# Kernel tuning notes

Measured on AMD Instinct MI355X. Metric: run time of the kernel, lower is better.

## Reference

```python
import jax, jax.numpy as jnp
import numpy as np

H = 4          # num attention heads
C1 = 64        # channel_num[0]
C2 = 128       # channel_num[1]
KV = C1 + C2   # 192
MLP = C1 * 4   # expand_ratio=4


def _layernorm(x, g, b, eps=1e-6):
    m = jnp.mean(x, axis=-1, keepdims=True)
    v = jnp.mean((x - m) ** 2, axis=-1, keepdims=True)
    return (x - m) * jax.lax.rsqrt(v + eps) * g + b


def setup_inputs() -> dict:
    key = jax.random.key(0)
    ks = jax.random.split(key, 12)
    B, N = 8, 3136
    s_q = 1.0 / np.sqrt(C1)
    s_kv = 1.0 / np.sqrt(KV)
    return {
        "emb1": jax.random.normal(ks[0], (B, N, C1), jnp.float32),
        "emb2": jax.random.normal(ks[1], (B, N, C2), jnp.float32),
        # per-head projection weights (nn.Linear convention: y = x @ W.T)
        "Wq": jax.random.uniform(ks[2], (H, C1, C1), jnp.float32, -s_q, s_q),
        "Wk": jax.random.uniform(ks[3], (H, KV, KV), jnp.float32, -s_kv, s_kv),
        "Wv": jax.random.uniform(ks[4], (H, KV, KV), jnp.float32, -s_kv, s_kv),
        "Wout": jax.random.uniform(ks[5], (C1, C1), jnp.float32, -s_q, s_q),
        "ln1_g": jnp.ones((C1,), jnp.float32),
        "ln1_b": jnp.zeros((C1,), jnp.float32),
        "lnall_g": jnp.ones((KV,), jnp.float32),
        "lnall_b": jnp.zeros((KV,), jnp.float32),
        "ffn_g": jnp.ones((C1,), jnp.float32),
        "ffn_b": jnp.zeros((C1,), jnp.float32),
        "fc1_w": jax.random.uniform(ks[6], (MLP, C1), jnp.float32, -s_q, s_q),
        "fc1_b": jnp.zeros((MLP,), jnp.float32),
        "fc2_w": jax.random.uniform(ks[7], (C1, MLP), jnp.float32, -1.0 / np.sqrt(MLP), 1.0 / np.sqrt(MLP)),
        "fc2_b": jnp.zeros((C1,), jnp.float32),
    }


def reference(emb1, emb2, Wq, Wk, Wv, Wout, ln1_g, ln1_b, lnall_g, lnall_b,
              ffn_g, ffn_b, fc1_w, fc1_b, fc2_w, fc2_b):
    # emb1: [B,N,C1], emb2: [B,N,C2]
    emb_all = jnp.concatenate([emb1, emb2], axis=2)          # [B,N,KV]
    cx1 = _layernorm(emb1, ln1_g, ln1_b)                     # [B,N,C1]
    ea = _layernorm(emb_all, lnall_g, lnall_b)               # [B,N,KV]

    # batched per-head projections (replaces Python loop over ModuleList)
    qT = jnp.einsum('bnc,hdc->bhdn', cx1, Wq)                # [B,H,C1,N]
    k = jnp.einsum('bnk,hdk->bhnd', ea, Wk)                  # [B,H,N,KV]
    vT = jnp.einsum('bnk,hdk->bhdn', ea, Wv)                 # [B,H,KV,N]

    scores = jnp.einsum('bhcn,bhnk->bhck', qT, k) / np.sqrt(KV)  # [B,H,C1,KV]
    # InstanceNorm2d over spatial dims (C1, KV) per (batch, head), affine=False
    m = jnp.mean(scores, axis=(2, 3), keepdims=True)
    v = jnp.mean((scores - m) ** 2, axis=(2, 3), keepdims=True)
    scores = (scores - m) * jax.lax.rsqrt(v + 1e-5)
    probs = jax.nn.softmax(scores, axis=3)                   # softmax over KV

    ctx = jnp.einsum('bhck,bhkn->bhcn', probs, vT)           # [B,H,C1,N]
    ctx = jnp.mean(ctx, axis=1).transpose(0, 2, 1)           # mean over heads -> [B,N,C1]
    o = ctx @ Wout.T                                         # [B,N,C1]

    cx = emb1 + o                                            # residual
    x = _layernorm(cx, ffn_g, ffn_b)
    x = jax.nn.gelu(x @ fc1_w.T + fc1_b, approximate=False)
    x = x @ fc2_w.T + fc2_b
    return x + cx
```

## Files before the change

kernel.cpp:

```cpp
#include <hip/hip_runtime.h>
#include <hip/hip_bf16.h>

typedef __hip_bfloat16 bf;
typedef unsigned short ushort_t;
typedef __attribute__((ext_vector_type(8))) short short8;
typedef __attribute__((ext_vector_type(4))) float f32x4;

#define NB 8
#define SEQ 3136
#define HD 4

__device__ __forceinline__ float lo_bf(unsigned u){ return __uint_as_float(u << 16); }
__device__ __forceinline__ float hi_bf(unsigned u){ return __uint_as_float(u & 0xffff0000u); }
__device__ __forceinline__ float b16f(ushort_t s){ return __uint_as_float(((unsigned)s) << 16); }
__device__ __forceinline__ unsigned short f2bfbits(float f){
  unsigned u = __float_as_uint(f);
  unsigned r = u + 0x7fffu + ((u >> 16) & 1u);
  return (unsigned short)(r >> 16);
}
__device__ __forceinline__ float ldin(const void* p, long i, bool isbf){
  return isbf ? __bfloat162float(((const bf*)p)[i]) : ((const float*)p)[i];
}
__device__ __forceinline__ float4 ld4(const void* p, long i, bool isbf){
  if (isbf){
    uint2 u = *reinterpret_cast<const uint2*>((const unsigned short*)p + i);
    return make_float4(lo_bf(u.x), hi_bf(u.x), lo_bf(u.y), hi_bf(u.y));
  }
  const float* f = (const float*)p + i;
  return make_float4(f[0], f[1], f[2], f[3]);
}
__device__ __forceinline__ short8 ldfrag(const void* p, long i, bool isbf){
  if (isbf) return *reinterpret_cast<const short8*>((const unsigned short*)p + i);
  const float* f = (const float*)p + i;
  short8 r;
  #pragma unroll
  for (int q=0;q<8;++q) r[q] = (short)f2bfbits(f[q]);
  return r;
}
#define DTYPE_FLAG(p) (((const unsigned*)(p))[0] == 0x3F803F80u)

__device__ __forceinline__ float wsum(float v){
  #pragma unroll
  for (int o = 32; o > 0; o >>= 1) v += __shfl_xor(v, o, 64);
  return v;
}
__device__ __forceinline__ float wmax(float v){
  #pragma unroll
  for (int o = 32; o > 0; o >>= 1) v = fmaxf(v, __shfl_xor(v, o, 64));
  return v;
}
__device__ __forceinline__ float gelu_f(float v){
  float u = v*(0.7978845608f + 0.0356774081f*v*v);
  return v * __builtin_amdgcn_rcpf(1.f + __expf(-2.f*u));
}

__global__ __launch_bounds__(256) void k_g(
    const void* __restrict__ emb1, const void* __restrict__ emb2,
    const void* __restrict__ g1, const void* __restrict__ b1,
    const void* __restrict__ ga, const void* __restrict__ ba,
    ushort_t* __restrict__ part, ushort_t* __restrict__ eag){
  bool isbf = DTYPE_FLAG(g1);
  __shared__ __align__(16) ushort_t z1t[64*40];
  __shared__ __align__(16) ushort_t zat[192*40];
  int tid = threadIdx.x, wave = tid >> 6, lane = tid & 63;
  int quad = lane >> 4, nl = lane & 15;
  int b = blockIdx.y, ch = blockIdx.x;
  long t0 = (long)b*SEQ + ch*32;
  float g1l = ldin(g1,lane,isbf), b1l = ldin(b1,lane,isbf);
  float ga0 = ldin(ga,lane,isbf),     ba0 = ldin(ba,lane,isbf);
  float ga1 = ldin(ga,64+lane,isbf),  ba1 = ldin(ba,64+lane,isbf);
  float ga2 = ldin(ga,128+lane,isbf), ba2 = ldin(ba,128+lane,isbf);
  #pragma unroll
  for (int k = 0; k < 8; ++k){
    int tok = wave*8 + k;
    long t = t0 + tok;
    float e1  = ldin(emb1, t*64 + lane, isbf);
    float e2a = ldin(emb2, t*128 + lane, isbf);
    float e2b = ldin(emb2, t*128 + 64 + lane, isbf);
    float s1 = wsum(e1), ss1 = wsum(e1*e1);
    float m1 = s1*(1.f/64.f);
    float r1 = rsqrtf(fmaxf(ss1*(1.f/64.f) - m1*m1, 0.f) + 1e-6f);
    z1t[lane*40 + tok] = f2bfbits((e1 - m1)*r1*g1l + b1l);
    float s23 = wsum(e2a+e2b), ss23 = wsum(e2a*e2a + e2b*e2b);
    float ma = (s1+s23)*(1.f/192.f);
    float ra = rsqrtf(fmaxf((ss1+ss23)*(1.f/192.f) - ma*ma, 0.f) + 1e-6f);
    unsigned short za0 = f2bfbits((e1  - ma)*ra*ga0 + ba0);
    unsigned short za1 = f2bfbits((e2a - ma)*ra*ga1 + ba1);
    unsigned short za2 = f2bfbits((e2b - ma)*ra*ga2 + ba2);
    zat[lane*40 + tok]       = za0;
    zat[(64+lane)*40 + tok]  = za1;
    zat[(128+lane)*40 + tok] = za2;
    eag[t*192 + lane]       = za0;
    eag[t*192 + 64 + lane]  = za1;
    eag[t*192 + 128 + lane] = za2;
  }
  __syncthreads();
  short8 a0 = *reinterpret_cast<const short8*>(&z1t[(wave*16+nl)*40 + quad*8]);
  ushort_t* P = part + ((long)b*98 + ch)*12288;
  #pragma unroll
  for (int nt = 0; nt < 12; ++nt){
    f32x4 cd = {0.f,0.f,0.f,0.f};
    short8 b0 = *reinterpret_cast<const short8*>(&zat[(nt*16+nl)*40 + quad*8]);
    cd = __builtin_amdgcn_mfma_f32_16x16x32_bf16(a0, b0, cd, 0, 0, 0);
    #pragma unroll
    for (int reg = 0; reg < 4; ++reg)
      P[(wave*16 + quad*4 + reg)*192 + nt*16 + nl] = f2bfbits(cd[reg]);
  }
}

__global__ __launch_bounds__(64) void k_red(
    const ushort_t* __restrict__ part, float* __restrict__ G){
  int idx4 = blockIdx.x*64 + threadIdx.x;
  int b = idx4 / 3072, e4 = idx4 - b*3072;
  const ushort_t* p = part + (long)b*98*12288 + e4*4;
  float s0=0.f, s1=0.f, s2=0.f, s3=0.f;
  #pragma unroll 2
  for (int ch = 0; ch < 98; ++ch){
    uint2 u = *reinterpret_cast<const uint2*>(p + (long)ch*12288);
    s0 += lo_bf(u.x); s1 += hi_bf(u.x); s2 += lo_bf(u.y); s3 += hi_bf(u.y);
  }
  ((float4*)G)[idx4] = make_float4(s0,s1,s2,s3);
}

__global__ __launch_bounds__(256) void k_s(
    const float* __restrict__ G, const void* __restrict__ Wq, const void* __restrict__ Wk,
    const void* __restrict__ lng, float* __restrict__ S){
  bool isbf = DTYPE_FLAG(lng);
  __shared__ __align__(16) ushort_t sGb[64*200];
  __shared__ __align__(16) ushort_t sT[48*72];
  int ec = blockIdx.x, h = blockIdx.y, b = blockIdx.z;
  int e0 = ec*48;
  int tid = threadIdx.x, wave = tid >> 6, lane = tid & 63;
  int quad = lane >> 4, nl = lane & 15;
  const float4* Gb4 = (const float4*)(G + (long)b*12288);
  for (int i16 = tid; i16 < 3072; i16 += 256){
    float4 v = Gb4[i16];
    int e = i16*4; int c = e/192, j = e - c*192;
    unsigned lo = (unsigned)f2bfbits(v.x) | ((unsigned)f2bfbits(v.y) << 16);
    unsigned hi = (unsigned)f2bfbits(v.z) | ((unsigned)f2bfbits(v.w) << 16);
    *reinterpret_cast<uint2*>(&sGb[c*200 + j]) = make_uint2(lo, hi);
  }
  __syncthreads();
  long wk0 = (long)h*36864;
  short8 aG[6];
  #pragma unroll
  for (int ks = 0; ks < 6; ++ks)
    aG[ks] = *reinterpret_cast<const short8*>(&sGb[(wave*16+nl)*200 + ks*32 + quad*8]);
  #pragma unroll
  for (int nt = 0; nt < 3; ++nt){
    f32x4 cd = {0.f,0.f,0.f,0.f};
    #pragma unroll
    for (int ks = 0; ks < 6; ++ks){
      short8 bw = ldfrag(Wk, wk0 + (long)(e0 + nt*16+nl)*192 + ks*32 + quad*8, isbf);
      cd = __builtin_amdgcn_mfma_f32_16x16x32_bf16(aG[ks], bw, cd, 0, 0, 0);
    }
    #pragma unroll
    for (int reg = 0; reg < 4; ++reg)
      sT[(nt*16+nl)*72 + wave*16 + quad*4 + reg] = f2bfbits(cd[reg]);
  }
  __syncthreads();
  long wq0 = (long)h*4096;
  short8 aQ[2];
  #pragma unroll
  for (int ks = 0; ks < 2; ++ks)
    aQ[ks] = ldfrag(Wq, wq0 + (long)(wave*16+nl)*64 + ks*32 + quad*8, isbf);
  const float scale = 0.07216878364870323f;
  float* Sb = S + ((long)b*HD + h)*12288;
  #pragma unroll
  for (int nt = 0; nt < 3; ++nt){
    f32x4 cd = {0.f,0.f,0.f,0.f};
    #pragma unroll
    for (int ks = 0; ks < 2; ++ks){
      short8 bt = *reinterpret_cast<const short8*>(&sT[(nt*16+nl)*72 + ks*32 + quad*8]);
      cd = __builtin_amdgcn_mfma_f32_16x16x32_bf16(aQ[ks], bt, cd, 0, 0, 0);
    }
    #pragma unroll
    for (int reg = 0; reg < 4; ++reg)
      Sb[(wave*16 + quad*4 + reg)*192 + e0 + nt*16 + nl] = cd[reg]*scale;
  }
}

__global__ __launch_bounds__(256) void k_smpv(
    const float* __restrict__ S, const void* __restrict__ Wv,
    const void* __restrict__ lng, float* __restrict__ Mh){
  bool isbf = DTYPE_FLAG(lng);
  __shared__ __align__(16) float sP[64*196];
  __shared__ __align__(16) unsigned sWv[192*52];
  __shared__ float red[8];
  __shared__ float stat[2];
  int jc = blockIdx.x, h = blockIdx.y, b = blockIdx.z;
  const float* Sb = S + ((long)b*HD + h)*12288;
  int tid = threadIdx.x, wave = tid >> 6, lane = tid & 63;
  long wv0 = (long)h*36864;
  float ps = 0.f, pss = 0.f;
  const float4* Sb4 = (const float4*)Sb;
  for (int i16 = tid; i16 < 3072; i16 += 256){
    float4 v = Sb4[i16];
    int e = i16*4; int c = e/192, j = e - c*192;
    *reinterpret_cast<float4*>(&sP[c*196 + j]) = v;
    ps += v.x + v.y + v.z + v.w;
    pss += v.x*v.x + v.y*v.y + v.z*v.z + v.w*v.w;
  }
  if (isbf){
    const unsigned short* wvp = (const unsigned short*)Wv + wv0 + jc*96;
    for (int idx = tid; idx < 4608; idx += 256){
      int r = idx/24, c2 = idx - r*24;
      uint2 v = *reinterpret_cast<const uint2*>(wvp + (long)r*192 + c2*4);
      *reinterpret_cast<uint2*>(&sWv[r*52 + c2*2]) = v;
    }
  } else {
    for (int idx = tid; idx < 9216; idx += 256){
      int r = idx/48, c = idx - r*48;
      float a0 = ldin(Wv, wv0 + (long)r*192 + jc*96 + c*2,     false);
      float a1 = ldin(Wv, wv0 + (long)r*192 + jc*96 + c*2 + 1, false);
      sWv[r*52 + c] = (unsigned)f2bfbits(a0) | ((unsigned)f2bfbits(a1) << 16);
    }
  }
  ps = wsum(ps); pss = wsum(pss);
  if (lane == 0){ red[wave] = ps; red[4+wave] = pss; }
  __syncthreads();
  if (tid == 0){
    float s  = red[0]+red[1]+red[2]+red[3];
    float s2 = red[4]+red[5]+red[6]+red[7];
    float m = s * (1.f/12288.f);
    stat[0] = m;
    stat[1] = rsqrtf(fmaxf(s2*(1.f/12288.f) - m*m, 0.f) + 1e-5f);
  }
  __syncthreads();
  float m = stat[0], r = stat[1];
  for (int rr = 0; rr < 16; ++rr){
    int row = wave*16 + rr;
    float v0 = (sP[row*196+lane]     - m)*r;
    float v1 = (sP[row*196+64+lane]  - m)*r;
    float v2 = (sP[row*196+128+lane] - m)*r;
    float mx = wmax(fmaxf(v0, fmaxf(v1, v2)));
    float e0 = __expf(v0-mx), e1 = __expf(v1-mx), e2 = __expf(v2-mx);
    float inv = 1.f / wsum(e0+e1+e2);
    sP[row*196+lane]     = e0*inv;
    sP[row*196+64+lane]  = e1*inv;
    sP[row*196+128+lane] = e2*inv;
  }
  __syncthreads();
  int ty = tid >> 4, tx = tid & 15;
  int j0 = jc*96 + tx*6;
  float acc[4][6];
  #pragma unroll
  for (int i=0;i<4;++i) for (int q=0;q<6;++q) acc[i][q]=0.f;
  #pragma unroll 2
  for (int e = 0; e < 192; ++e){
    float p4[4];
    #pragma unroll
    for (int i=0;i<4;++i) p4[i] = sP[(ty*4+i)*196 + e];
    unsigned wa = sWv[e*52 + tx*3];
    unsigned wb = sWv[e*52 + tx*3 + 1];
    unsigned wc = sWv[e*52 + tx*3 + 2];
    float w0 = lo_bf(wa), w1 = hi_bf(wa), w2 = lo_bf(wb),
          w3 = hi_bf(wb), w4 = lo_bf(wc), w5 = hi_bf(wc);
    #pragma unroll
    for (int i=0;i<4;++i){
      acc[i][0] = fmaf(p4[i], w0, acc[i][0]);
      acc[i][1] = fmaf(p4[i], w1, acc[i][1]);
      acc[i][2] = fmaf(p4[i], w2, acc[i][2]);
      acc[i][3] = fmaf(p4[i], w3, acc[i][3]);
      acc[i][4] = fmaf(p4[i], w4, acc[i][4]);
      acc[i][5] = fmaf(p4[i], w5, acc[i][5]);
    }
  }
  float* Mb = Mh + ((long)b*HD + h)*12288;
  #pragma unroll
  for (int i=0;i<4;++i)
    #pragma unroll
    for (int q=0;q<6;++q)
      Mb[(ty*4+i)*192 + j0 + q] = acc[i][q];
}

__global__ __launch_bounds__(256) void k_w2(
    const float* __restrict__ Mh, const void* __restrict__ Wout,
    const void* __restrict__ lng, ushort_t* __restrict__ W2){
  bool isbf = DTYPE_FLAG(lng);
  __shared__ __align__(16) float sM[64*49];
  int jc = blockIdx.x, b = blockIdx.y;
  int tid = threadIdx.x;
  for (int idx = tid; idx < 3072; idx += 256){
    int c = idx/48, j = idx - c*48;
    long base = (long)b*HD*12288 + c*192 + jc*48 + j;
    float s = Mh[base] + Mh[base+12288] + Mh[base+2*12288] + Mh[base+3*12288];
    sM[c*49 + j] = 0.25f*s;
  }
  __syncthreads();
  int ty = tid >> 4, tx = tid & 15;
  float acc[4][3];
  #pragma unroll
  for (int i=0;i<4;++i) for (int q=0;q<3;++q) acc[i][q]=0.f;
  for (int c = 0; c < 64; c += 4){
    float4 w4[4];
    #pragma unroll
    for (int i=0;i<4;++i) w4[i] = ld4(Wout, (long)(ty*4+i)*64 + c, isbf);
    float ww[4][4];
    #pragma unroll
    for (int i=0;i<4;++i){ ww[i][0]=w4[i].x; ww[i][1]=w4[i].y; ww[i][2]=w4[i].z; ww[i][3]=w4[i].w; }
    #pragma unroll
    for (int u = 0; u < 4; ++u){
      float t3[3];
      #pragma unroll
      for (int q=0;q<3;++q) t3[q] = sM[(c+u)*49 + tx*3 + q];
      #pragma unroll
      for (int i=0;i<4;++i)
        #pragma unroll
        for (int q=0;q<3;++q) acc[i][q] = fmaf(ww[i][u], t3[q], acc[i][q]);
    }
  }
  ushort_t* W2b = W2 + (long)b*12288;
  #pragma unroll
  for (int i=0;i<4;++i)
    #pragma unroll
    for (int q=0;q<3;++q)
      W2b[(ty*4+i)*192 + jc*48 + tx*3 + q] = f2bfbits(acc[i][q]);
}

__global__ __launch_bounds__(256) void k_tail(
    const void* __restrict__ emb1, const ushort_t* __restrict__ eag,
    const ushort_t* __restrict__ W2g,
    const void* __restrict__ ffg, const void* __restrict__ ffb,
    const void* __restrict__ f1w, const void* __restrict__ f1b,
    const void* __restrict__ f2w, const void* __restrict__ f2b,
    const void* __restrict__ lng, void* __restrict__ out){
  bool isbf = DTYPE_FLAG(lng);
  __shared__ __align__(16) ushort_t sCX[32*72];
  __shared__ __align__(16) ushort_t sX[32*88];
  __shared__ __align__(16) ushort_t sH[32*280];
  int tid = threadIdx.x, wave = tid >> 6, lane = tid & 63;
  int quad = lane >> 4, nl = lane & 15;
  int b = blockIdx.y;
  long tbase = (long)b*SEQ + blockIdx.x*32;

  short8 aO[2][6];
  #pragma unroll
  for (int tt = 0; tt < 2; ++tt)
    #pragma unroll
    for (int kt = 0; kt < 6; ++kt)
      aO[tt][kt] = *reinterpret_cast<const short8*>(eag + (tbase + tt*16 + nl)*192 + kt*32 + quad*8);
  const ushort_t* W2b = W2g + (long)b*12288;
  short8 bW[6];
  #pragma unroll
  for (int kt = 0; kt < 6; ++kt)
    bW[kt] = *reinterpret_cast<const short8*>(W2b + (wave*16+nl)*192 + kt*32 + quad*8);
  short8 bF1[8];
  #pragma unroll
  for (int nn = 0; nn < 4; ++nn)
    #pragma unroll
    for (int kt = 0; kt < 2; ++kt)
      bF1[nn*2+kt] = ldfrag(f1w, (long)((wave*4+nn)*16+nl)*64 + kt*32 + quad*8, isbf);
  short8 bF2[8];
  #pragma unroll
  for (int kt = 0; kt < 8; ++kt)
    bF2[kt] = ldfrag(f2w, (long)(wave*16+nl)*256 + kt*32 + quad*8, isbf);
  float e1v[2][4];
  #pragma unroll
  for (int tt = 0; tt < 2; ++tt)
    #pragma unroll
    for (int reg = 0; reg < 4; ++reg)
      e1v[tt][reg] = ldin(emb1, (tbase + tt*16 + quad*4 + reg)*64 + wave*16 + nl, isbf);
  float gl = ldin(ffg, lane, isbf), bl = ldin(ffb, lane, isbf);
  float f1bb[4];
  #pragma unroll
  for (int nn = 0; nn < 4; ++nn) f1bb[nn] = ldin(f1b, (wave*4+nn)*16+nl, isbf);
  float f2bb = ldin(f2b, wave*16+nl, isbf);

  #pragma unroll
  for (int tt = 0; tt < 2; ++tt){
    f32x4 cd = {0.f,0.f,0.f,0.f};
    #pragma unroll
    for (int kt = 0; kt < 6; ++kt)
      cd = __builtin_amdgcn_mfma_f32_16x16x32_bf16(aO[tt][kt], bW[kt], cd, 0, 0, 0);
    #pragma unroll
    for (int reg = 0; reg < 4; ++reg){
      int tokl = tt*16 + quad*4 + reg;
      sCX[tokl*72 + wave*16 + nl] = f2bfbits(cd[reg] + e1v[tt][reg]);
    }
  }
  __syncthreads();

  #pragma unroll
  for (int k = 0; k < 8; ++k){
    int tokl = wave*8 + k;
    float c = b16f(sCX[tokl*72 + lane]);
    float s = wsum(c), ss = wsum(c*c);
    float m = s*(1.f/64.f);
    float r = rsqrtf(fmaxf(ss*(1.f/64.f) - m*m, 0.f) + 1e-6f);
    sX[tokl*88 + lane] = f2bfbits((c - m)*r*gl + bl);
  }
  __syncthreads();

  short8 aX[2][2];
  #pragma unroll
  for (int tt = 0; tt < 2; ++tt)
    #pragma unroll
    for (int kt = 0; kt < 2; ++kt)
      aX[tt][kt] = *reinterpret_cast<const short8*>(&sX[(tt*16+nl)*88 + kt*32 + quad*8]);
  #pragma unroll
  for (int tt = 0; tt < 2; ++tt){
    #pragma unroll
    for (int nn = 0; nn < 4; ++nn){
      int nt = wave*4 + nn;
      f32x4 cd = {0.f,0.f,0.f,0.f};
      #pragma unroll
      for (int kt = 0; kt < 2; ++kt)
        cd = __builtin_amdgcn_mfma_f32_16x16x32_bf16(aX[tt][kt], bF1[nn*2+kt], cd, 0, 0, 0);
      #pragma unroll
      for (int reg = 0; reg < 4; ++reg)
        sH[(tt*16 + quad*4 + reg)*280 + nt*16 + nl] = f2bfbits(gelu_f(cd[reg] + f1bb[nn]));
    }
  }
  __syncthreads();

  short8 aH[2][8];
  #pragma unroll
  for (int tt = 0; tt < 2; ++tt)
    #pragma unroll
    for (int kt = 0; kt < 8; ++kt)
      aH[tt][kt] = *reinterpret_cast<const short8*>(&sH[(tt*16+nl)*280 + kt*32 + quad*8]);
  #pragma unroll
  for (int tt = 0; tt < 2; ++tt){
    f32x4 cd = {0.f,0.f,0.f,0.f};
    #pragma unroll
    for (int kt = 0; kt < 8; ++kt)
      cd = __builtin_amdgcn_mfma_f32_16x16x32_bf16(aH[tt][kt], bF2[kt], cd, 0, 0, 0);
    #pragma unroll
    for (int reg = 0; reg < 4; ++reg){
      int tokl = tt*16 + quad*4 + reg;
      int chn = wave*16 + nl;
      float y = cd[reg] + f2bb + b16f(sCX[tokl*72 + chn]);
      if (isbf) sCX[tokl*72 + chn] = f2bfbits(y);
      else ((float*)out)[(tbase + tokl)*64 + chn] = y;
    }
  }
  if (isbf){
    __syncthreads();
    #pragma unroll
    for (int pp = 0; pp < 2; ++pp){
      int tokl = wave*8 + pp*4 + (lane >> 4), prt = lane & 15;
      uint2 v = *reinterpret_cast<const uint2*>(&sCX[tokl*72 + prt*4]);
      *reinterpret_cast<uint2*>((ushort_t*)out + (tbase + tokl)*64 + prt*4) = v;
    }
  }
}

extern "C" void kernel_launch(void* const* d_in, const int* in_sizes, int n_in,
                              void* d_out, int out_size, void* d_ws, size_t ws_size,
                              hipStream_t stream){
  const void* emb1 = d_in[0];
  const void* emb2 = d_in[1];
  const void* Wq   = d_in[2];
  const void* Wk   = d_in[3];
  const void* Wv   = d_in[4];
  const void* Wout = d_in[5];
  const void* ln1g = d_in[6];
  const void* ln1b = d_in[7];
  const void* lag  = d_in[8];
  const void* lab  = d_in[9];
  const void* ffg  = d_in[10];
  const void* ffb  = d_in[11];
  const void* f1w  = d_in[12];
  const void* f1b  = d_in[13];
  const void* f2w  = d_in[14];
  const void* f2b  = d_in[15];

  char* base = (char*)d_ws;
  ushort_t* part = (ushort_t*)base;
  ushort_t* ea   = (ushort_t*)(base + 19267584);
  float*    G    = (float*)(base + 28901376);
  float*    S    = (float*)(base + 29294592);
  float*    Mh   = (float*)(base + 30867456);
  ushort_t* W2   = (ushort_t*)(base + 32440320);

  k_g   <<<dim3(98,NB),   256, 0, stream>>>(emb1, emb2, ln1g, ln1b, lag, lab, part, ea);
  k_red <<<384,            64, 0, stream>>>(part, G);
  k_s   <<<dim3(4,HD,NB), 256, 0, stream>>>(G, Wq, Wk, ln1g, S);
  k_smpv<<<dim3(2,HD,NB), 256, 0, stream>>>(S, Wv, ln1g, Mh);
  k_w2  <<<dim3(4,NB),    256, 0, stream>>>(Mh, Wout, ln1g, W2);
  k_tail<<<dim3(98,NB),   256, 0, stream>>>(emb1, ea, W2, ffg, ffb,
                                            f1w, f1b, f2w, f2b, ln1g, d_out);
}
```

Before: 211.7 us.

## Fuse all stages into one cooperative persistent kernel with grid syncs

Replaces six separate kernel launches with a single cooperative kernel of 512 blocks that runs each stage in turn, separated by grid-wide barriers, and keeps the old multi-kernel path as a fallback if the cooperative launch fails. The Gram-partial stage also now covers 64 tokens per block instead of 32, which halves the partial buffer and the reduction work. The goal is to remove launch gaps and the inter-kernel drain between the small middle stages. In exchange, the tail stage runs on 512 persistent blocks looping over 784 tiles, so the work is unevenly split, and the 64KB static shared allocation may limit occupancy and make the grid syncs costly.

```diff
diff --git a/kernel.cpp b/kernel.cpp
--- a/kernel.cpp
+++ b/kernel.cpp
@@ -1,5 +1,7 @@
 #include <hip/hip_runtime.h>
 #include <hip/hip_bf16.h>
+#include <hip/hip_cooperative_groups.h>
+namespace cg = cooperative_groups;
 
 typedef __hip_bfloat16 bf;
 typedef unsigned short ushort_t;
@@ -54,25 +56,419 @@
   return v * __builtin_amdgcn_rcpf(1.f + __expf(-2.f*u));
 }
 
+__global__ __launch_bounds__(256) void k_all(
+    const void* __restrict__ emb1, const void* __restrict__ emb2,
+    const void* __restrict__ Wq,   const void* __restrict__ Wk,
+    const void* __restrict__ Wv,   const void* __restrict__ Wout,
+    const void* __restrict__ ln1g, const void* __restrict__ ln1b,
+    const void* __restrict__ lag,  const void* __restrict__ lab,
+    const void* __restrict__ ffg,  const void* __restrict__ ffb,
+    const void* __restrict__ f1w,  const void* __restrict__ f1b,
+    const void* __restrict__ f2w,  const void* __restrict__ f2b,
+    ushort_t* __restrict__ part, ushort_t* __restrict__ eag,
+    float* __restrict__ G, float* __restrict__ S, float* __restrict__ Mh,
+    ushort_t* __restrict__ W2, void* __restrict__ out){
+  cg::grid_group grid = cg::this_grid();
+  bool isbf = DTYPE_FLAG(ln1g);
+  __shared__ __align__(16) unsigned char smem[65536];
+  __shared__ float red[8];
+  __shared__ float stat[2];
+  int bid = blockIdx.x;
+  int tid = threadIdx.x, wave = tid >> 6, lane = tid & 63;
+  int quad = lane >> 4, nl = lane & 15;
+
+  if (bid < 392){
+    ushort_t* z1t = (ushort_t*)smem;
+    ushort_t* zat = (ushort_t*)(smem + 9216);
+    int ch = bid % 49, b = bid / 49;
+    long t0 = (long)b*SEQ + ch*64;
+    float g1l = ldin(ln1g,lane,isbf), b1l = ldin(ln1b,lane,isbf);
+    float ga0 = ldin(lag,lane,isbf),     ba0 = ldin(lab,lane,isbf);
+    float ga1 = ldin(lag,64+lane,isbf),  ba1 = ldin(lab,64+lane,isbf);
+    float ga2 = ldin(lag,128+lane,isbf), ba2 = ldin(lab,128+lane,isbf);
+    #pragma unroll 4
+    for (int k = 0; k < 16; ++k){
+      int tok = wave*16 + k;
+      long t = t0 + tok;
+      float e1  = ldin(emb1, t*64 + lane, isbf);
+      float e2a = ldin(emb2, t*128 + lane, isbf);
+      float e2b = ldin(emb2, t*128 + 64 + lane, isbf);
+      float s1 = wsum(e1), ss1 = wsum(e1*e1);
+      float m1 = s1*(1.f/64.f);
+      float r1 = rsqrtf(fmaxf(ss1*(1.f/64.f) - m1*m1, 0.f) + 1e-6f);
+      z1t[lane*72 + tok] = f2bfbits((e1 - m1)*r1*g1l + b1l);
+      float s23 = wsum(e2a+e2b), ss23 = wsum(e2a*e2a + e2b*e2b);
+      float ma = (s1+s23)*(1.f/192.f);
+      float ra = rsqrtf(fmaxf((ss1+ss23)*(1.f/192.f) - ma*ma, 0.f) + 1e-6f);
+      unsigned short za0 = f2bfbits((e1  - ma)*ra*ga0 + ba0);
+      unsigned short za1 = f2bfbits((e2a - ma)*ra*ga1 + ba1);
+      unsigned short za2 = f2bfbits((e2b - ma)*ra*ga2 + ba2);
+      zat[lane*72 + tok]       = za0;
+      zat[(64+lane)*72 + tok]  = za1;
+      zat[(128+lane)*72 + tok] = za2;
+      eag[t*192 + lane]       = za0;
+      eag[t*192 + 64 + lane]  = za1;
+      eag[t*192 + 128 + lane] = za2;
+    }
+    __syncthreads();
+    short8 a0 = *reinterpret_cast<const short8*>(&z1t[(wave*16+nl)*72 + quad*8]);
+    short8 a1 = *reinterpret_cast<const short8*>(&z1t[(wave*16+nl)*72 + 32 + quad*8]);
+    ushort_t* P = part + ((long)b*49 + ch)*12288;
+    #pragma unroll
+    for (int nt = 0; nt < 12; ++nt){
+      f32x4 cd = {0.f,0.f,0.f,0.f};
+      short8 b0 = *reinterpret_cast<const short8*>(&zat[(nt*16+nl)*72 + quad*8]);
+      cd = __builtin_amdgcn_mfma_f32_16x16x32_bf16(a0, b0, cd, 0, 0, 0);
+      short8 b1v = *reinterpret_cast<const short8*>(&zat[(nt*16+nl)*72 + 32 + quad*8]);
+      cd = __builtin_amdgcn_mfma_f32_16x16x32_bf16(a1, b1v, cd, 0, 0, 0);
+      #pragma unroll
+      for (int reg = 0; reg < 4; ++reg)
+        P[(wave*16 + quad*4 + reg)*192 + nt*16 + nl] = f2bfbits(cd[reg]);
+    }
+  }
+  grid.sync();
+
+  {
+    int idx4 = bid*256 + tid;
+    if (idx4 < 24576){
+      int b = idx4 / 3072, e4 = idx4 - b*3072;
+      const ushort_t* p = part + (long)b*49*12288 + e4*4;
+      float s0=0.f, s1=0.f, s2=0.f, s3=0.f;
+      #pragma unroll
+      for (int ch = 0; ch < 49; ++ch){
+        uint2 u = *reinterpret_cast<const uint2*>(p + (long)ch*12288);
+        s0 += lo_bf(u.x); s1 += hi_bf(u.x); s2 += lo_bf(u.y); s3 += hi_bf(u.y);
+      }
+      ((float4*)G)[idx4] = make_float4(s0,s1,s2,s3);
+    }
+  }
+  grid.sync();
+
+  if (bid < 128){
+    ushort_t* sGb = (ushort_t*)smem;
+    ushort_t* sT  = (ushort_t*)(smem + 25600);
+    int ec = bid & 3, h = (bid >> 2) & 3, b = bid >> 4;
+    int e0 = ec*48;
+    const float4* Gb4 = (const float4*)(G + (long)b*12288);
+    for (int i16 = tid; i16 < 3072; i16 += 256){
+      float4 v = Gb4[i16];
+      int e = i16*4; int c = e/192, j = e - c*192;
+      unsigned lo = (unsigned)f2bfbits(v.x) | ((unsigned)f2bfbits(v.y) << 16);
+      unsigned hi = (unsigned)f2bfbits(v.z) | ((unsigned)f2bfbits(v.w) << 16);
+      *reinterpret_cast<uint2*>(&sGb[c*200 + j]) = make_uint2(lo, hi);
+    }
+    __syncthreads();
+    long wk0 = (long)h*36864;
+    short8 aG[6];
+    #pragma unroll
+    for (int ks = 0; ks < 6; ++ks)
+      aG[ks] = *reinterpret_cast<const short8*>(&sGb[(wave*16+nl)*200 + ks*32 + quad*8]);
+    #pragma unroll
+    for (int nt = 0; nt < 3; ++nt){
+      f32x4 cd = {0.f,0.f,0.f,0.f};
+      #pragma unroll
+      for (int ks = 0; ks < 6; ++ks){
+        short8 bw = ldfrag(Wk, wk0 + (long)(e0 + nt*16+nl)*192 + ks*32 + quad*8, isbf);
+        cd = __builtin_amdgcn_mfma_f32_16x16x32_bf16(aG[ks], bw, cd, 0, 0, 0);
+      }
+      #pragma unroll
+      for (int reg = 0; reg < 4; ++reg)
+        sT[(nt*16+nl)*72 + wave*16 + quad*4 + reg] = f2bfbits(cd[reg]);
+    }
+    __syncthreads();
+    long wq0 = (long)h*4096;
+    short8 aQ[2];
+    #pragma unroll
+    for (int ks = 0; ks < 2; ++ks)
+      aQ[ks] = ldfrag(Wq, wq0 + (long)(wave*16+nl)*64 + ks*32 + quad*8, isbf);
+    const float scale = 0.07216878364870323f;
+    float* Sb = S + ((long)b*HD + h)*12288;
+    #pragma unroll
+    for (int nt = 0; nt < 3; ++nt){
+      f32x4 cd = {0.f,0.f,0.f,0.f};
+      #pragma unroll
+      for (int ks = 0; ks < 2; ++ks){
+        short8 bt = *reinterpret_cast<const short8*>(&sT[(nt*16+nl)*72 + ks*32 + quad*8]);
+        cd = __builtin_amdgcn_mfma_f32_16x16x32_bf16(aQ[ks], bt, cd, 0, 0, 0);
+      }
+      #pragma unroll
+      for (int reg = 0; reg < 4; ++reg)
+        Sb[(wave*16 + quad*4 + reg)*192 + e0 + nt*16 + nl] = cd[reg]*scale;
+    }
+  }
+  grid.sync();
+
+  if (bid < 64){
+    ushort_t* sPb = (ushort_t*)smem;
+    unsigned* sWv = (unsigned*)(smem + 25600);
+    int jc = bid & 1, h = (bid >> 1) & 3, b = bid >> 3;
+    const float* Sb = S + ((long)b*HD + h)*12288;
+    long wv0 = (long)h*36864;
+    float ps = 0.f, pss = 0.f;
+    const float4* Sb4 = (const float4*)Sb;
+    for (int i16 = tid; i16 < 3072; i16 += 256){
+      float4 v = Sb4[i16];
+      int e = i16*4; int c = e/192, j = e - c*192;
+      ps += v.x + v.y + v.z + v.w;
+      pss += v.x*v.x + v.y*v.y + v.z*v.z + v.w*v.w;
+      unsigned lo = (unsigned)f2bfbits(v.x) | ((unsigned)f2bfbits(v.y) << 16);
+      unsigned hi = (unsigned)f2bfbits(v.z) | ((unsigned)f2bfbits(v.w) << 16);
+      *reinterpret_cast<uint2*>(&sPb[c*200 + j]) = make_uint2(lo, hi);
+    }
+    if (isbf){
+      const unsigned short* wvp = (const unsigned short*)Wv + wv0 + jc*96;
+      for (int idx = tid; idx < 4608; idx += 256){
+        int r = idx/24, c2 = idx - r*24;
+        uint2 v = *reinterpret_cast<const uint2*>(wvp + (long)r*192 + c2*4);
+        *reinterpret_cast<uint2*>(&sWv[r*52 + c2*2]) = v;
+      }
+    } else {
+      for (int idx = tid; idx < 9216; idx += 256){
+        int r = idx/48, c = idx - r*48;
+        float a0 = ldin(Wv, wv0 + (long)r*192 + jc*96 + c*2,     false);
+        float a1 = ldin(Wv, wv0 + (long)r*192 + jc*96 + c*2 + 1, false);
+        sWv[r*52 + c] = (unsigned)f2bfbits(a0) | ((unsigned)f2bfbits(a1) << 16);
+      }
+    }
+    ps = wsum(ps); pss = wsum(pss);
+    if (lane == 0){ red[wave] = ps; red[4+wave] = pss; }
+    __syncthreads();
+    if (tid == 0){
+      float s  = red[0]+red[1]+red[2]+red[3];
+      float s2 = red[4]+red[5]+red[6]+red[7];
+      float m = s * (1.f/12288.f);
+      stat[0] = m;
+      stat[1] = rsqrtf(fmaxf(s2*(1.f/12288.f) - m*m, 0.f) + 1e-5f);
+    }
+    __syncthreads();
+    float m = stat[0], r = stat[1];
+    for (int rr = 0; rr < 16; ++rr){
+      int row = wave*16 + rr;
+      float v0 = (b16f(sPb[row*200+lane])     - m)*r;
+      float v1 = (b16f(sPb[row*200+64+lane])  - m)*r;
+      float v2 = (b16f(sPb[row*200+128+lane]) - m)*r;
+      float mx = wmax(fmaxf(v0, fmaxf(v1, v2)));
+      float e0 = __expf(v0-mx), e1 = __expf(v1-mx), e2 = __expf(v2-mx);
+      float inv = 1.f / wsum(e0+e1+e2);
+      sPb[row*200+lane]     = f2bfbits(e0*inv);
+      sPb[row*200+64+lane]  = f2bfbits(e1*inv);
+      sPb[row*200+128+lane] = f2bfbits(e2*inv);
+    }
+    __syncthreads();
+    int ty = tid >> 4, tx = tid & 15;
+    int j0 = jc*96 + tx*6;
+    float acc[4][6];
+    #pragma unroll
+    for (int i=0;i<4;++i) for (int q=0;q<6;++q) acc[i][q]=0.f;
+    #pragma unroll 2
+    for (int e = 0; e < 192; ++e){
+      float p4[4];
+      #pragma unroll
+      for (int i=0;i<4;++i) p4[i] = b16f(sPb[(ty*4+i)*200 + e]);
+      unsigned wa = sWv[e*52 + tx*3];
+      unsigned wb = sWv[e*52 + tx*3 + 1];
+      unsigned wc = sWv[e*52 + tx*3 + 2];
+      float w0 = lo_bf(wa), w1 = hi_bf(wa), w2 = lo_bf(wb),
+            w3 = hi_bf(wb), w4 = lo_bf(wc), w5 = hi_bf(wc);
+      #pragma unroll
+      for (int i=0;i<4;++i){
+        acc[i][0] = fmaf(p4[i], w0, acc[i][0]);
+        acc[i][1] = fmaf(p4[i], w1, acc[i][1]);
+        acc[i][2] = fmaf(p4[i], w2, acc[i][2]);
+        acc[i][3] = fmaf(p4[i], w3, acc[i][3]);
+        acc[i][4] = fmaf(p4[i], w4, acc[i][4]);
+        acc[i][5] = fmaf(p4[i], w5, acc[i][5]);
+      }
+    }
+    float* Mb = Mh + ((long)b*HD + h)*12288;
+    #pragma unroll
+    for (int i=0;i<4;++i)
+      #pragma unroll
+      for (int q=0;q<6;++q)
+        Mb[(ty*4+i)*192 + j0 + q] = acc[i][q];
+  }
+  grid.sync();
+
+  if (bid < 32){
+    float* sM = (float*)smem;
+    int jc = bid & 3, b = bid >> 2;
+    for (int idx = tid; idx < 3072; idx += 256){
+      int c = idx/48, j = idx - c*48;
+      long base = (long)b*HD*12288 + c*192 + jc*48 + j;
+      float s = Mh[base] + Mh[base+12288] + Mh[base+2*12288] + Mh[base+3*12288];
+      sM[c*49 + j] = 0.25f*s;
+    }
+    __syncthreads();
+    int ty = tid >> 4, tx = tid & 15;
+    float acc[4][3];
+    #pragma unroll
+    for (int i=0;i<4;++i) for (int q=0;q<3;++q) acc[i][q]=0.f;
+    for (int c = 0; c < 64; c += 4){
+      float4 w4[4];
+      #pragma unroll
+      for (int i=0;i<4;++i) w4[i] = ld4(Wout, (long)(ty*4+i)*64 + c, isbf);
+      float ww[4][4];
+      #pragma unroll
+      for (int i=0;i<4;++i){ ww[i][0]=w4[i].x; ww[i][1]=w4[i].y; ww[i][2]=w4[i].z; ww[i][3]=w4[i].w; }
+      #pragma unroll
+      for (int u = 0; u < 4; ++u){
+        float t3[3];
+        #pragma unroll
+        for (int q=0;q<3;++q) t3[q] = sM[(c+u)*49 + tx*3 + q];
+        #pragma unroll
+        for (int i=0;i<4;++i)
+          #pragma unroll
+          for (int q=0;q<3;++q) acc[i][q] = fmaf(ww[i][u], t3[q], acc[i][q]);
+      }
+    }
+    ushort_t* W2b = W2 + (long)b*12288;
+    #pragma unroll
+    for (int i=0;i<4;++i)
+      #pragma unroll
+      for (int q=0;q<3;++q)
+        W2b[(ty*4+i)*192 + jc*48 + tx*3 + q] = f2bfbits(acc[i][q]);
+  }
+  grid.sync();
+
+  {
+    ushort_t* sCX = (ushort_t*)smem;
+    ushort_t* sX  = (ushort_t*)(smem + 4608);
+    ushort_t* sH  = (ushort_t*)(smem + 10240);
+    float gl = ldin(ffg, lane, isbf), bl = ldin(ffb, lane, isbf);
+    float f1bb[4];
+    #pragma unroll
+    for (int nn = 0; nn < 4; ++nn) f1bb[nn] = ldin(f1b, (wave*4+nn)*16+nl, isbf);
+    float f2bb = ldin(f2b, wave*16+nl, isbf);
+    short8 bF1[8];
+    #pragma unroll
+    for (int nn = 0; nn < 4; ++nn)
+      #pragma unroll
+      for (int kt = 0; kt < 2; ++kt)
+        bF1[nn*2+kt] = ldfrag(f1w, (long)((wave*4+nn)*16+nl)*64 + kt*32 + quad*8, isbf);
+    short8 bF2[8];
+    #pragma unroll
+    for (int kt = 0; kt < 8; ++kt)
+      bF2[kt] = ldfrag(f2w, (long)(wave*16+nl)*256 + kt*32 + quad*8, isbf);
+
+    for (int u = bid; u < 784; u += 512){
+      int tile = u % 98, b = u / 98;
+      long tbase = (long)b*SEQ + tile*32;
+      short8 aO[2][6];
+      #pragma unroll
+      for (int tt = 0; tt < 2; ++tt)
+        #pragma unroll
+        for (int kt = 0; kt < 6; ++kt)
+          aO[tt][kt] = *reinterpret_cast<const short8*>(eag + (tbase + tt*16 + nl)*192 + kt*32 + quad*8);
+      const ushort_t* W2b = W2 + (long)b*12288;
+      short8 bW[6];
+      #pragma unroll
+      for (int kt = 0; kt < 6; ++kt)
+        bW[kt] = *reinterpret_cast<const short8*>(W2b + (wave*16+nl)*192 + kt*32 + quad*8);
+      float e1v[2][4];
+      #pragma unroll
+      for (int tt = 0; tt < 2; ++tt)
+        #pragma unroll
+        for (int reg = 0; reg < 4; ++reg)
+          e1v[tt][reg] = ldin(emb1, (tbase + tt*16 + quad*4 + reg)*64 + wave*16 + nl, isbf);
+
+      #pragma unroll
+      for (int tt = 0; tt < 2; ++tt){
+        f32x4 cd = {0.f,0.f,0.f,0.f};
+        #pragma unroll
+        for (int kt = 0; kt < 6; ++kt)
+          cd = __builtin_amdgcn_mfma_f32_16x16x32_bf16(aO[tt][kt], bW[kt], cd, 0, 0, 0);
+        #pragma unroll
+        for (int reg = 0; reg < 4; ++reg){
+          int tokl = tt*16 + quad*4 + reg;
+          sCX[tokl*72 + wave*16 + nl] = f2bfbits(cd[reg] + e1v[tt][reg]);
+        }
+      }
+      __syncthreads();
+      #pragma unroll
+      for (int k = 0; k < 8; ++k){
+        int tokl = wave*8 + k;
+        float c = b16f(sCX[tokl*72 + lane]);
+        float s = wsum(c), ss = wsum(c*c);
+        float m = s*(1.f/64.f);
+        float r = rsqrtf(fmaxf(ss*(1.f/64.f) - m*m, 0.f) + 1e-6f);
+        sX[tokl*88 + lane] = f2bfbits((c - m)*r*gl + bl);
+      }
+      __syncthreads();
+      short8 aX[2][2];
+      #pragma unroll
+      for (int tt = 0; tt < 2; ++tt)
+        #pragma unroll
+        for (int kt = 0; kt < 2; ++kt)
+          aX[tt][kt] = *reinterpret_cast<const short8*>(&sX[(tt*16+nl)*88 + kt*32 + quad*8]);
+      #pragma unroll
+      for (int tt = 0; tt < 2; ++tt){
+        #pragma unroll
+        for (int nn = 0; nn < 4; ++nn){
+          int nt = wave*4 + nn;
+          f32x4 cd = {0.f,0.f,0.f,0.f};
+          #pragma unroll
+          for (int kt = 0; kt < 2; ++kt)
+            cd = __builtin_amdgcn_mfma_f32_16x16x32_bf16(aX[tt][kt], bF1[nn*2+kt], cd, 0, 0, 0);
+          #pragma unroll
+          for (int reg = 0; reg < 4; ++reg)
+            sH[(tt*16 + quad*4 + reg)*280 + nt*16 + nl] = f2bfbits(gelu_f(cd[reg] + f1bb[nn]));
+        }
+      }
+      __syncthreads();
+      short8 aH[2][8];
+      #pragma unroll
+      for (int tt = 0; tt < 2; ++tt)
+        #pragma unroll
+        for (int kt = 0; kt < 8; ++kt)
+          aH[tt][kt] = *reinterpret_cast<const short8*>(&sH[(tt*16+nl)*280 + kt*32 + quad*8]);
+      #pragma unroll
+      for (int tt = 0; tt < 2; ++tt){
+        f32x4 cd = {0.f,0.f,0.f,0.f};
+        #pragma unroll
+        for (int kt = 0; kt < 8; ++kt)
+          cd = __builtin_amdgcn_mfma_f32_16x16x32_bf16(aH[tt][kt], bF2[kt], cd, 0, 0, 0);
+        #pragma unroll
+        for (int reg = 0; reg < 4; ++reg){
+          int tokl = tt*16 + quad*4 + reg;
+          int chn = wave*16 + nl;
+          float y = cd[reg] + f2bb + b16f(sCX[tokl*72 + chn]);
+          if (isbf) sCX[tokl*72 + chn] = f2bfbits(y);
+          else ((float*)out)[(tbase + tokl)*64 + chn] = y;
+        }
+      }
+      __syncthreads();
+      if (isbf){
+        #pragma unroll
+        for (int pp = 0; pp < 2; ++pp){
+          int tokl = wave*8 + pp*4 + (lane >> 4), prt = lane & 15;
+          uint2 v = *reinterpret_cast<const uint2*>(&sCX[tokl*72 + prt*4]);
+          *reinterpret_cast<uint2*>((ushort_t*)out + (tbase + tokl)*64 + prt*4) = v;
+        }
+      }
+      __syncthreads();
+    }
+  }
+}
+
 __global__ __launch_bounds__(256) void k_g(
     const void* __restrict__ emb1, const void* __restrict__ emb2,
     const void* __restrict__ g1, const void* __restrict__ b1,
     const void* __restrict__ ga, const void* __restrict__ ba,
     ushort_t* __restrict__ part, ushort_t* __restrict__ eag){
   bool isbf = DTYPE_FLAG(g1);
-  __shared__ __align__(16) ushort_t z1t[64*40];
-  __shared__ __align__(16) ushort_t zat[192*40];
+  __shared__ __align__(16) ushort_t z1t[64*72];
+  __shared__ __align__(16) ushort_t zat[192*72];
   int tid = threadIdx.x, wave = tid >> 6, lane = tid & 63;
   int quad = lane >> 4, nl = lane & 15;
   int b = blockIdx.y, ch = blockIdx.x;
-  long t0 = (long)b*SEQ + ch*32;
+  long t0 = (long)b*SEQ + ch*64;
   float g1l = ldin(g1,lane,isbf), b1l = ldin(b1,lane,isbf);
   float ga0 = ldin(ga,lane,isbf),     ba0 = ldin(ba,lane,isbf);
   float ga1 = ldin(ga,64+lane,isbf),  ba1 = ldin(ba,64+lane,isbf);
   float ga2 = ldin(ga,128+lane,isbf), ba2 = ldin(ba,128+lane,isbf);
-  #pragma unroll
-  for (int k = 0; k < 8; ++k){
-    int tok = wave*8 + k;
+  #pragma unroll 4
+  for (int k = 0; k < 16; ++k){
+    int tok = wave*16 + k;
     long t = t0 + tok;
     float e1  = ldin(emb1, t*64 + lane, isbf);
     float e2a = ldin(emb2, t*128 + lane, isbf);
@@ -80,28 +476,31 @@
     float s1 = wsum(e1), ss1 = wsum(e1*e1);
     float m1 = s1*(1.f/64.f);
     float r1 = rsqrtf(fmaxf(ss1*(1.f/64.f) - m1*m1, 0.f) + 1e-6f);
-    z1t[lane*40 + tok] = f2bfbits((e1 - m1)*r1*g1l + b1l);
+    z1t[lane*72 + tok] = f2bfbits((e1 - m1)*r1*g1l + b1l);
     float s23 = wsum(e2a+e2b), ss23 = wsum(e2a*e2a + e2b*e2b);
     float ma = (s1+s23)*(1.f/192.f);
     float ra = rsqrtf(fmaxf((ss1+ss23)*(1.f/192.f) - ma*ma, 0.f) + 1e-6f);
     unsigned short za0 = f2bfbits((e1  - ma)*ra*ga0 + ba0);
     unsigned short za1 = f2bfbits((e2a - ma)*ra*ga1 + ba1);
     unsigned short za2 = f2bfbits((e2b - ma)*ra*ga2 + ba2);
-    zat[lane*40 + tok]       = za0;
-    zat[(64+lane)*40 + tok]  = za1;
-    zat[(128+lane)*40 + tok] = za2;
+    zat[lane*72 + tok]       = za0;
+    zat[(64+lane)*72 + tok]  = za1;
+    zat[(128+lane)*72 + tok] = za2;
     eag[t*192 + lane]       = za0;
     eag[t*192 + 64 + lane]  = za1;
     eag[t*192 + 128 + lane] = za2;
   }
   __syncthreads();
-  short8 a0 = *reinterpret_cast<const short8*>(&z1t[(wave*16+nl)*40 + quad*8]);
-  ushort_t* P = part + ((long)b*98 + ch)*12288;
+  short8 a0 = *reinterpret_cast<const short8*>(&z1t[(wave*16+nl)*72 + quad*8]);
+  short8 a1 = *reinterpret_cast<const short8*>(&z1t[(wave*16+nl)*72 + 32 + quad*8]);
+  ushort_t* P = part + ((long)b*49 + ch)*12288;
   #pragma unroll
   for (int nt = 0; nt < 12; ++nt){
     f32x4 cd = {0.f,0.f,0.f,0.f};
-    short8 b0 = *reinterpret_cast<const short8*>(&zat[(nt*16+nl)*40 + quad*8]);
+    short8 b0 = *reinterpret_cast<const short8*>(&zat[(nt*16+nl)*72 + quad*8]);
     cd = __builtin_amdgcn_mfma_f32_16x16x32_bf16(a0, b0, cd, 0, 0, 0);
+    short8 b1v = *reinterpret_cast<const short8*>(&zat[(nt*16+nl)*72 + 32 + quad*8]);
+    cd = __builtin_amdgcn_mfma_f32_16x16x32_bf16(a1, b1v, cd, 0, 0, 0);
     #pragma unroll
     for (int reg = 0; reg < 4; ++reg)
       P[(wave*16 + quad*4 + reg)*192 + nt*16 + nl] = f2bfbits(cd[reg]);
@@ -112,10 +511,10 @@
     const ushort_t* __restrict__ part, float* __restrict__ G){
   int idx4 = blockIdx.x*64 + threadIdx.x;
   int b = idx4 / 3072, e4 = idx4 - b*3072;
-  const ushort_t* p = part + (long)b*98*12288 + e4*4;
+  const ushort_t* p = part + (long)b*49*12288 + e4*4;
   float s0=0.f, s1=0.f, s2=0.f, s3=0.f;
-  #pragma unroll 2
-  for (int ch = 0; ch < 98; ++ch){
+  #pragma unroll
+  for (int ch = 0; ch < 49; ++ch){
     uint2 u = *reinterpret_cast<const uint2*>(p + (long)ch*12288);
     s0 += lo_bf(u.x); s1 += hi_bf(u.x); s2 += lo_bf(u.y); s3 += hi_bf(u.y);
   }
@@ -333,7 +732,6 @@
   int quad = lane >> 4, nl = lane & 15;
   int b = blockIdx.y;
   long tbase = (long)b*SEQ + blockIdx.x*32;
-
   short8 aO[2][6];
   #pragma unroll
   for (int tt = 0; tt < 2; ++tt)
@@ -366,7 +764,6 @@
   #pragma unroll
   for (int nn = 0; nn < 4; ++nn) f1bb[nn] = ldin(f1b, (wave*4+nn)*16+nl, isbf);
   float f2bb = ldin(f2b, wave*16+nl, isbf);
-
   #pragma unroll
   for (int tt = 0; tt < 2; ++tt){
     f32x4 cd = {0.f,0.f,0.f,0.f};
@@ -380,7 +777,6 @@
     }
   }
   __syncthreads();
-
   #pragma unroll
   for (int k = 0; k < 8; ++k){
     int tokl = wave*8 + k;
@@ -391,7 +787,6 @@
     sX[tokl*88 + lane] = f2bfbits((c - m)*r*gl + bl);
   }
   __syncthreads();
-
   short8 aX[2][2];
   #pragma unroll
   for (int tt = 0; tt < 2; ++tt)
@@ -413,7 +808,6 @@
     }
   }
   __syncthreads();
-
   short8 aH[2][8];
   #pragma unroll
   for (int tt = 0; tt < 2; ++tt)
@@ -468,17 +862,28 @@
 
   char* base = (char*)d_ws;
   ushort_t* part = (ushort_t*)base;
-  ushort_t* ea   = (ushort_t*)(base + 19267584);
-  float*    G    = (float*)(base + 28901376);
-  float*    S    = (float*)(base + 29294592);
-  float*    Mh   = (float*)(base + 30867456);
-  ushort_t* W2   = (ushort_t*)(base + 32440320);
-
-  k_g   <<<dim3(98,NB),   256, 0, stream>>>(emb1, emb2, ln1g, ln1b, lag, lab, part, ea);
-  k_red <<<384,            64, 0, stream>>>(part, G);
-  k_s   <<<dim3(4,HD,NB), 256, 0, stream>>>(G, Wq, Wk, ln1g, S);
-  k_smpv<<<dim3(2,HD,NB), 256, 0, stream>>>(S, Wv, ln1g, Mh);
-  k_w2  <<<dim3(4,NB),    256, 0, stream>>>(Mh, Wout, ln1g, W2);
-  k_tail<<<dim3(98,NB),   256, 0, stream>>>(emb1, ea, W2, ffg, ffb,
-                                            f1w, f1b, f2w, f2b, ln1g, d_out);
-}
+  ushort_t* ea   = (ushort_t*)(base + 9633792);
+  float*    G    = (float*)(base + 19267584);
+  float*    S    = (float*)(base + 19660800);
+  float*    Mh   = (float*)(base + 21233664);
+  ushort_t* W2   = (ushort_t*)(base + 22806528);
+
+  void* args[] = {
+    (void*)&emb1, (void*)&emb2, (void*)&Wq, (void*)&Wk, (void*)&Wv, (void*)&Wout,
+    (void*)&ln1g, (void*)&ln1b, (void*)&lag, (void*)&lab, (void*)&ffg, (void*)&ffb,
+    (void*)&f1w, (void*)&f1b, (void*)&f2w, (void*)&f2b,
+    (void*)&part, (void*)&ea, (void*)&G, (void*)&S, (void*)&Mh, (void*)&W2,
+    (void*)&d_out
+  };
+  hipError_t err = hipLaunchCooperativeKernel((const void*)k_all, dim3(512), dim3(256),
+                                              args, 0, stream);
+  if (err != hipSuccess){
+    k_g   <<<dim3(49,NB),   256, 0, stream>>>(emb1, emb2, ln1g, ln1b, lag, lab, part, ea);
+    k_red <<<384,            64, 0, stream>>>(part, G);
+    k_s   <<<dim3(4,HD,NB), 256, 0, stream>>>(G, Wq, Wk, ln1g, S);
+    k_smpv<<<dim3(2,HD,NB), 256, 0, stream>>>(S, Wv, ln1g, Mh);
+    k_w2  <<<dim3(4,NB),    256, 0, stream>>>(Mh, Wout, ln1g, W2);
+    k_tail<<<dim3(98,NB),   256, 0, stream>>>(emb1, ea, W2, ffg, ffb,
+                                              f1w, f1b, f2w, f2b, ln1g, d_out);
+  }
+}
```

Result: slower. 496.9 us (+134.7%).
